# Kernel optimization log

Measured on AMD Instinct MI355X. Metric: run time of the kernel, lower is better.

The kernel has to match this reference:

```python
import jax, jax.numpy as jnp
import numpy as np

B, S, D = 8, 4096, 256
H, DK, DV = 8, 32, 32


def _layer_norm(x, g, b, eps=1e-6):
    mu = jnp.mean(x, axis=-1, keepdims=True)
    var = jnp.mean(jnp.square(x - mu), axis=-1, keepdims=True)
    return (x - mu) * jax.lax.rsqrt(var + eps) * g + b


def setup_inputs() -> dict:
    key = jax.random.key(0)
    ks = jax.random.split(key, 16)
    std = 1.0 / np.sqrt(D)
    p = lambda k, shp: (jax.random.normal(k, shp, jnp.float32) * std)
    return {
        "h": jax.random.normal(ks[0], (B, S, D), jnp.float32),
        "e": jax.random.normal(ks[1], (B, S, D), jnp.float32),
        "s": jax.random.normal(ks[2], (B, D), jnp.float32),
        "sat_wq": p(ks[3], (D, H * DK)), "sat_wk": p(ks[4], (D, H * DK)),
        "sat_wv": p(ks[5], (D, H * DV)), "sat_wo": p(ks[6], (H * DV, D)),
        "sat_g": jnp.ones((D,), jnp.float32), "sat_b": jnp.zeros((D,), jnp.float32),
        "rel_wq": p(ks[7], (D, H * DK)), "rel_wk": p(ks[8], (D, H * DK)),
        "rel_wv": p(ks[9], (D, H * DV)), "rel_wo": p(ks[10], (H * DV, D)),
        "rel_g": jnp.ones((D,), jnp.float32), "rel_b": jnp.zeros((D,), jnp.float32),
    }


def reference(h, e, s, sat_wq, sat_wk, sat_wv, sat_wo, sat_g, sat_b,
              rel_wq, rel_wk, rel_wv, rel_wo, rel_g, rel_b):
    b, sl, d = h.shape
    scale = 1.0 / np.sqrt(DK)

    # ---- build 5-token context: [left, self, right, entity, relay] ----
    hp = jnp.pad(h, ((0, 0), (1, 1), (0, 0)))  # zeros at both ends
    s_exp = jnp.broadcast_to(s[:, None, :], (b, sl, d))
    ctx = jnp.stack([hp[:, :sl], h, hp[:, 2:], e, s_exp], axis=2)  # [B,S,5,D]

    # ---- satellite attention: 1 query vs 5-token context per position ----
    q = (h @ sat_wq).reshape(b, sl, H, DK)
    k = (ctx @ sat_wk).reshape(b, sl, 5, H, DK)
    v = (ctx @ sat_wv).reshape(b, sl, 5, H, DV)
    attn = jax.nn.softmax(jnp.einsum('bshd,bschd->bshc', q, k) * scale, axis=-1)
    o = jnp.einsum('bshc,bschd->bshd', attn, v).reshape(b, sl, H * DV) @ sat_wo
    h_out = _layer_norm(o + h, sat_g, sat_b)  # [B,S,D]

    # ---- relay attention: relay query vs [s; h_out] ----
    s_h = jnp.concatenate([s[:, None, :], h_out], axis=1)  # [B,S+1,D]
    qr = (s @ rel_wq).reshape(b, H, DK)
    kr = (s_h @ rel_wk).reshape(b, sl + 1, H, DK)
    vr = (s_h @ rel_wv).reshape(b, sl + 1, H, DV)
    attn_r = jax.nn.softmax(jnp.einsum('bhd,bkhd->bhk', qr, kr) * scale, axis=-1)
    orl = jnp.einsum('bhk,bkhd->bhd', attn_r, vr).reshape(b, H * DV) @ rel_wo
    s_out = _layer_norm(orl + s, rel_g, rel_b)  # [B,D]

    return (h_out, s_out)
```

## Files before the change

### kernel.cpp

```cpp
#include <hip/hip_runtime.h>
#include <hip/hip_bf16.h>

typedef unsigned short ushort_t;
typedef unsigned int uint_t;
typedef __attribute__((ext_vector_type(8))) short bf16x8;
typedef __attribute__((ext_vector_type(4))) float f32x4;

#define NB 8
#define NS 4096
#define ND 256
#define NH 8
#define NDK 32
#define NBS (NB*NS)
#define NK  (NS+1)
#define CH  513
#define NCH 8
static const size_t PBUF = (size_t)NB*(NS+1)*ND;
static const size_t HSZ  = (size_t)NBS*ND;

__device__ __forceinline__ ushort_t f2b(float x){
  union { __hip_bfloat16 b; ushort_t u; } cv; cv.b = __float2bfloat16(x); return cv.u;
}
__device__ __forceinline__ float b2f(ushort_t u){
  union { uint_t u; float f; } cv; cv.u = ((uint_t)u) << 16; return cv.f;
}
__device__ __forceinline__ void gload16(const ushort_t* g, ushort_t* l){
  __builtin_amdgcn_global_load_lds(
      (const __attribute__((address_space(1))) void*)g,
      (__attribute__((address_space(3))) void*)l, 16, 0, 0);
}
__device__ __forceinline__ uint4 packbf16x8(float4 a, float4 b){
  uint4 p;
  p.x = f2b(a.x) | ((uint_t)f2b(a.y)<<16);
  p.y = f2b(a.z) | ((uint_t)f2b(a.w)<<16);
  p.z = f2b(b.x) | ((uint_t)f2b(b.y)<<16);
  p.w = f2b(b.z) | ((uint_t)f2b(b.w)<<16);
  return p;
}

__device__ __forceinline__ float bsum256(float v){
  __shared__ float tmp[4];
  #pragma unroll
  for (int o=32;o>0;o>>=1) v += __shfl_down(v,o);
  if ((threadIdx.x & 63)==0) tmp[threadIdx.x>>6] = v;
  __syncthreads();
  float r = tmp[0]+tmp[1]+tmp[2]+tmp[3];
  __syncthreads();
  return r;
}

__global__ __launch_bounds__(256) void prep(
    const float* __restrict__ w0, const float* __restrict__ w1, const float* __restrict__ w2,
    const float* __restrict__ w3, const float* __restrict__ w4, const float* __restrict__ w5,
    ushort_t* __restrict__ WtAll,
    const float* __restrict__ s,
    const float* __restrict__ rwq,
    ushort_t* __restrict__ ksb, ushort_t* __restrict__ vsb,
    float* __restrict__ qr, ushort_t* __restrict__ krv)
{
  __shared__ float sh[64*68];
  const int blk = blockIdx.x;
  const int tid = threadIdx.x;
  if (blk < 96){
    const int z = blk >> 4, xy = blk & 15;
    const float* W = (z==0)?w0:(z==1)?w1:(z==2)?w2:(z==3)?w3:(z==4)?w4:w5;
    ushort_t* Wt = WtAll + (size_t)z*65536;
    float (*t)[68] = (float(*)[68])sh;
    const int k0 = (xy>>2)*64, n0 = (xy&3)*64;
    const int tr = tid>>4, tc4 = (tid&15)*4;
    #pragma unroll
    for (int i=0;i<4;i++){
      int r = tr + i*16;
      float4 v = *(const float4*)&W[(size_t)(k0+r)*ND + n0 + tc4];
      t[r][tc4]=v.x; t[r][tc4+1]=v.y; t[r][tc4+2]=v.z; t[r][tc4+3]=v.w;
    }
    __syncthreads();
    #pragma unroll
    for (int i=0;i<4;i++){
      int n = tr + i*16;
      uint_t q0 = f2b(t[tc4+0][n]) | ((uint_t)f2b(t[tc4+1][n])<<16);
      uint_t q1 = f2b(t[tc4+2][n]) | ((uint_t)f2b(t[tc4+3][n])<<16);
      *(uint2*)&Wt[(size_t)(n0+n)*ND + k0 + tc4] = make_uint2(q0,q1);
    }
  } else {
    const int rem = blk - 96;
    const int b = rem & 7, which = rem >> 3;
    const float* W = (which==0)?w1:(which==1)?w2:(which==2)?rwq:(which==3)?w4:w5;
    float* a = sh;
    a[tid] = s[(size_t)b*ND + tid];
    __syncthreads();
    float acc = 0.f;
    #pragma unroll 8
    for (int d=0; d<ND; d++)
      acc = fmaf(a[d], W[(size_t)d*ND + tid], acc);
    switch (which){
      case 0: ksb[(size_t)b*ND + tid] = f2b(acc); break;
      case 1: vsb[(size_t)b*ND + tid] = f2b(acc); break;
      case 2: qr[(size_t)b*ND + tid] = acc; break;
      case 3: krv[(size_t)b*NK*512 + tid] = f2b(acc); break;
      default: krv[(size_t)b*NK*512 + 256 + tid] = f2b(acc); break;
    }
  }
}

__global__ __launch_bounds__(512) void gemm_qkve(const float* __restrict__ hA,
    const float* __restrict__ eA, const ushort_t* __restrict__ Wt,
    ushort_t* __restrict__ hQKV, ushort_t* __restrict__ eKV)
{
  __shared__ __align__(16) ushort_t As[2][128][64];
  __shared__ __align__(16) ushort_t Bs[2][128][64];
  const int y = blockIdx.y;
  const float* A; const ushort_t* Wb; ushort_t* Y; int ldn, col0;
  if (y < 6){ A=hA; Wb=Wt;        Y=hQKV; ldn=768; col0=y*128; }
  else      { A=eA; Wb=Wt+65536;  Y=eKV;  ldn=512; col0=(y-6)*128; }
  const int tid  = threadIdx.x;
  const int row0 = blockIdx.x*128;
  const int lane = tid & 63;
  const int wave = tid >> 6;
  const int wr = (wave>>2)*64;
  const int wc = (wave&3)*32;
  const int l15 = lane & 15, lg = lane >> 4;
  const int lr8 = lane >> 3;
  const int l7  = lane & 7;
  const int ls  = l7 ^ lr8;

  const float* Af = A + (size_t)(row0 + wave*16 + lr8)*ND + l7*8;
  char* AwBase = (char*)&As[0][0][0];
  const int awoff = (wave*16 + lr8)*128 + ((l7 ^ lr8)<<4);
  const ushort_t* Bsrc = Wb + (size_t)(col0 + wave*16 + lr8)*ND + ls*8;

  f32x4 acc[4][2] = {};

  #define STAGE(t, bb) do{ \
    const float* ga = Af + (t)*64; \
    float4 a0=*(const float4*)ga,          a1=*(const float4*)(ga+4); \
    float4 a2=*(const float4*)(ga+8*ND),   a3=*(const float4*)(ga+8*ND+4); \
    *(uint4*)(AwBase + (size_t)(bb)*16384 + awoff)        = packbf16x8(a0,a1); \
    *(uint4*)(AwBase + (size_t)(bb)*16384 + awoff + 1024) = packbf16x8(a2,a3); \
    gload16(Bsrc + (t)*64,                &Bs[bb][wave*16][0]); \
    gload16(Bsrc + (size_t)8*ND + (t)*64, &Bs[bb][wave*16+8][0]); \
  }while(0)
  #define COMPUTE(bb) do{ \
    _Pragma("unroll") \
    for (int ks=0; ks<2; ks++){ \
      bf16x8 af[4], bfr[2]; \
      _Pragma("unroll") \
      for (int mi=0;mi<4;mi++){ \
        int ra = wr + mi*16 + l15; int cb = (ks<<6) + (lg<<4); \
        af[mi] = *(const bf16x8*)((const char*)&As[bb][0][0] + ra*128 + (cb ^ ((ra&7)<<4))); \
      } \
      _Pragma("unroll") \
      for (int ni=0;ni<2;ni++){ \
        int rb = wc + ni*16 + l15; int cb = (ks<<6) + (lg<<4); \
        bfr[ni] = *(const bf16x8*)((const char*)&Bs[bb][0][0] + rb*128 + (cb ^ ((rb&7)<<4))); \
      } \
      _Pragma("unroll") \
      for (int mi=0;mi<4;mi++) \
        _Pragma("unroll") \
        for (int ni=0;ni<2;ni++) \
          acc[mi][ni] = __builtin_amdgcn_mfma_f32_16x16x32_bf16(af[mi], bfr[ni], acc[mi][ni], 0,0,0); \
    } \
  }while(0)

  STAGE(0, 0);
  __syncthreads();
  STAGE(1, 1); COMPUTE(0); __syncthreads();
  STAGE(2, 0); COMPUTE(1); __syncthreads();
  STAGE(3, 1); COMPUTE(0); __syncthreads();
  COMPUTE(1);
  #undef STAGE
  #undef COMPUTE

  #pragma unroll
  for (int mi=0;mi<4;mi++)
    #pragma unroll
    for (int r=0;r<4;r++){
      size_t orow = (size_t)(row0 + wr + mi*16 + lg*4 + r);
      #pragma unroll
      for (int ni=0;ni<2;ni++)
        Y[orow*(size_t)ldn + col0 + wc + ni*16 + l15] = f2b(acc[mi][ni][r]);
    }
}

__global__ __launch_bounds__(512) void gemm_krv(const ushort_t* __restrict__ A,
    const ushort_t* __restrict__ Wt, ushort_t* __restrict__ Y)
{
  __shared__ __align__(16) ushort_t As[2][128][64];
  __shared__ __align__(16) ushort_t Bs[2][128][64];
  const int tid  = threadIdx.x;
  const int row0 = blockIdx.x*128;
  const int col0 = blockIdx.y*128;
  const int lane = tid & 63;
  const int wave = tid >> 6;
  const int wr = (wave>>2)*64;
  const int wc = (wave&3)*32;
  const int l15 = lane & 15, lg = lane >> 4;
  const int lr8 = lane >> 3;
  const int ls  = (lane & 7) ^ lr8;

  const ushort_t* Asrc = A  + (size_t)(row0 + wave*16 + lr8)*ND + ls*8;
  const ushort_t* Bsrc = Wt + (size_t)(col0 + wave*16 + lr8)*ND + ls*8;

  f32x4 acc[4][2] = {};

  #define STAGE(t, bb) do{ \
    gload16(Asrc + (t)*64,                &As[bb][wave*16][0]); \
    gload16(Asrc + (size_t)8*ND + (t)*64, &As[bb][wave*16+8][0]); \
    gload16(Bsrc + (t)*64,                &Bs[bb][wave*16][0]); \
    gload16(Bsrc + (size_t)8*ND + (t)*64, &Bs[bb][wave*16+8][0]); \
  }while(0)
  #define COMPUTE(bb) do{ \
    _Pragma("unroll") \
    for (int ks=0; ks<2; ks++){ \
      bf16x8 af[4], bfr[2]; \
      _Pragma("unroll") \
      for (int mi=0;mi<4;mi++){ \
        int ra = wr + mi*16 + l15; int cb = (ks<<6) + (lg<<4); \
        af[mi] = *(const bf16x8*)((const char*)&As[bb][0][0] + ra*128 + (cb ^ ((ra&7)<<4))); \
      } \
      _Pragma("unroll") \
      for (int ni=0;ni<2;ni++){ \
        int rb = wc + ni*16 + l15; int cb = (ks<<6) + (lg<<4); \
        bfr[ni] = *(const bf16x8*)((const char*)&Bs[bb][0][0] + rb*128 + (cb ^ ((rb&7)<<4))); \
      } \
      _Pragma("unroll") \
      for (int mi=0;mi<4;mi++) \
        _Pragma("unroll") \
        for (int ni=0;ni<2;ni++) \
          acc[mi][ni] = __builtin_amdgcn_mfma_f32_16x16x32_bf16(af[mi], bfr[ni], acc[mi][ni], 0,0,0); \
    } \
  }while(0)

  STAGE(0, 0);
  __syncthreads();
  STAGE(1, 1); COMPUTE(0); __syncthreads();
  STAGE(2, 0); COMPUTE(1); __syncthreads();
  STAGE(3, 1); COMPUTE(0); __syncthreads();
  COMPUTE(1);
  #undef STAGE
  #undef COMPUTE

  #pragma unroll
  for (int mi=0;mi<4;mi++)
    #pragma unroll
    for (int r=0;r<4;r++){
      int row = row0 + wr + mi*16 + lg*4 + r;
      size_t orow = (size_t)(row>>12)*NK + 1 + (row&4095);
      #pragma unroll
      for (int ni=0;ni<2;ni++)
        Y[orow*512 + col0 + wc + ni*16 + l15] = f2b(acc[mi][ni][r]);
    }
}

__global__ __launch_bounds__(512) void oproj_ln(const ushort_t* __restrict__ A,
    const ushort_t* __restrict__ Wt, const float* __restrict__ hres,
    const float* __restrict__ g, const float* __restrict__ bta,
    float* __restrict__ outf, ushort_t* __restrict__ outb)
{
  __shared__ __align__(16) ushort_t As[2][64][64];
  __shared__ float rs[64][4], rq[64][4];
  __shared__ float gl[ND], bl[ND];
  const int tid  = threadIdx.x;
  const int row0 = blockIdx.x*64;
  const int lane = tid & 63;
  const int wave = tid >> 6;
  const int wr = (wave>>2)*32;
  const int wc = (wave&3)*64;
  const int l15 = lane & 15, lg = lane >> 4;
  const int lr8 = lane >> 3;
  const int ls  = (lane & 7) ^ lr8;

  if (tid < ND){ gl[tid] = g[tid]; bl[tid] = bta[tid]; }

  const ushort_t* Asrc = A + (size_t)(row0 + wave*8 + lr8)*ND + ls*8;

  f32x4 acc[2][4] = {};

  #define STAGE3(t, bb) gload16(Asrc + (t)*64, &As[bb][wave*8][0])
  #define COMPUTE3(t, bb) do{ \
    _Pragma("unroll") \
    for (int ks=0; ks<2; ks++){ \
      bf16x8 af[2], bfr[4]; \
      _Pragma("unroll") \
      for (int mi=0;mi<2;mi++){ \
        int ra = wr + mi*16 + l15; int cb = (ks<<6) + (lg<<4); \
        af[mi] = *(const bf16x8*)((const char*)&As[bb][0][0] + ra*128 + (cb ^ ((ra&7)<<4))); \
      } \
      _Pragma("unroll") \
      for (int ni=0;ni<4;ni++) \
        bfr[ni] = *(const bf16x8*)&Wt[(size_t)(wc + ni*16 + l15)*ND + (t)*64 + ks*32 + lg*8]; \
      _Pragma("unroll") \
      for (int mi=0;mi<2;mi++) \
        _Pragma("unroll") \
        for (int ni=0;ni<4;ni++) \
          acc[mi][ni] = __builtin_amdgcn_mfma_f32_16x16x32_bf16(af[mi], bfr[ni], acc[mi][ni], 0,0,0); \
    } \
  }while(0)

  STAGE3(0, 0);
  __syncthreads();
  STAGE3(1, 1); COMPUTE3(0, 0); __syncthreads();
  STAGE3(2, 0); COMPUTE3(1, 1); __syncthreads();
  STAGE3(3, 1); COMPUTE3(2, 0); __syncthreads();
  COMPUTE3(3, 1);
  #undef STAGE3
  #undef COMPUTE3

  #pragma unroll
  for (int mi=0;mi<2;mi++)
    #pragma unroll
    for (int rr=0;rr<4;rr++){
      size_t rowb = (size_t)(row0 + wr + mi*16 + lg*4 + rr)*ND;
      #pragma unroll
      for (int ni=0;ni<4;ni++)
        acc[mi][ni][rr] += hres[rowb + wc + ni*16 + l15];
    }

  #pragma unroll
  for (int mi=0;mi<2;mi++)
    #pragma unroll
    for (int rr=0;rr<4;rr++){
      float sv = 0.f, qv = 0.f;
      #pragma unroll
      for (int ni=0;ni<4;ni++){ float x = acc[mi][ni][rr]; sv += x; qv += x*x; }
      #pragma unroll
      for (int o=1;o<16;o<<=1){ sv += __shfl_xor(sv,o); qv += __shfl_xor(qv,o); }
      if (l15 == 0){
        int rl = wr + mi*16 + lg*4 + rr;
        rs[rl][wave&3] = sv; rq[rl][wave&3] = qv;
      }
    }
  __syncthreads();

  #pragma unroll
  for (int mi=0;mi<2;mi++)
    #pragma unroll
    for (int rr=0;rr<4;rr++){
      int rl = wr + mi*16 + lg*4 + rr;
      float sm = rs[rl][0] + rs[rl][1] + rs[rl][2] + rs[rl][3];
      float sq = rq[rl][0] + rq[rl][1] + rq[rl][2] + rq[rl][3];
      float mu = sm * (1.0f/ND);
      float var = sq * (1.0f/ND) - mu*mu;
      float rstd = rsqrtf(var + 1e-6f);
      size_t rowb = (size_t)(row0 + rl)*ND;
      #pragma unroll
      for (int ni=0;ni<4;ni++){
        int col = wc + ni*16 + l15;
        float yv = (acc[mi][ni][rr] - mu)*rstd*gl[col] + bl[col];
        outf[rowb + col] = yv;
        outb[rowb + col] = f2b(yv);
      }
    }
}

__device__ __forceinline__ void load8(float* d, const ushort_t* p){
  bf16x8 v = *(const bf16x8*)p;
  #pragma unroll
  for (int i=0;i<8;i++) d[i] = b2f((ushort_t)v[i]);
}
__device__ __forceinline__ void zero8(float* d){
  #pragma unroll
  for (int i=0;i<8;i++) d[i] = 0.f;
}
__global__ __launch_bounds__(256) void sat_attn4(const ushort_t* __restrict__ HQ,
    const ushort_t* __restrict__ EKV,
    const ushort_t* __restrict__ KS, const ushort_t* __restrict__ VS,
    ushort_t* __restrict__ O)
{
  const int tid = threadIdx.x;
  const int l  = tid & 3;
  const int g  = tid >> 2;
  const int hh = g & 7;
  const int pi = g >> 3;
  const int pos = blockIdx.x*8 + pi;
  const int b = pos >> 12, t = pos & 4095;
  const int co = hh*NDK + l*8;
  const float scale = 0.17677669529663687f;

  const size_t rq = (size_t)pos*768;
  const size_t re = (size_t)pos*512;
  float q[8], k0[8], k1[8], k2[8], k3[8], k4[8];
  load8(q,  HQ + rq + co);
  load8(k1, HQ + rq + 256 + co);
  load8(k3, EKV + re + co);
  load8(k4, KS + (size_t)b*ND + co);
  if (t > 0)    load8(k0, HQ + rq - 768 + 256 + co);
  else          zero8(k0);
  if (t < NS-1) load8(k2, HQ + rq + 768 + 256 + co);
  else          zero8(k2);

  float s0=0.f,s1=0.f,s2=0.f,s3=0.f,s4=0.f;
  #pragma unroll
  for (int i=0;i<8;i++){
    s0 = fmaf(q[i],k0[i],s0); s1 = fmaf(q[i],k1[i],s1); s2 = fmaf(q[i],k2[i],s2);
    s3 = fmaf(q[i],k3[i],s3); s4 = fmaf(q[i],k4[i],s4);
  }
  #pragma unroll
  for (int mm=1; mm<4; mm<<=1){
    s0 += __shfl_xor(s0,mm); s1 += __shfl_xor(s1,mm); s2 += __shfl_xor(s2,mm);
    s3 += __shfl_xor(s3,mm); s4 += __shfl_xor(s4,mm);
  }
  s0*=scale; s1*=scale; s2*=scale; s3*=scale; s4*=scale;
  float m = fmaxf(fmaxf(fmaxf(s0,s1),fmaxf(s2,s3)),s4);
  float p0=expf(s0-m), p1=expf(s1-m), p2=expf(s2-m), p3=expf(s3-m), p4=expf(s4-m);
  float inv = 1.0f/(p0+p1+p2+p3+p4);

  float v0[8], v1[8], v2[8], v3[8], v4[8];
  load8(v1, HQ + rq + 512 + co);
  load8(v3, EKV + re + 256 + co);
  load8(v4, VS + (size_t)b*ND + co);
  if (t > 0)    load8(v0, HQ + rq - 768 + 512 + co);
  else          zero8(v0);
  if (t < NS-1) load8(v2, HQ + rq + 768 + 512 + co);
  else          zero8(v2);

  float o[8];
  #pragma unroll
  for (int i=0;i<8;i++)
    o[i] = (p0*v0[i] + p1*v1[i] + p2*v2[i] + p3*v3[i] + p4*v4[i]) * inv;
  uint4 pk;
  pk.x = f2b(o[0])|((uint_t)f2b(o[1])<<16);
  pk.y = f2b(o[2])|((uint_t)f2b(o[3])<<16);
  pk.z = f2b(o[4])|((uint_t)f2b(o[5])<<16);
  pk.w = f2b(o[6])|((uint_t)f2b(o[7])<<16);
  *(uint4*)&O[(size_t)pos*ND + co] = pk;
}

__global__ __launch_bounds__(256) void rel_part(const float* __restrict__ QR,
    const ushort_t* __restrict__ KRV,
    float* __restrict__ pO, float* __restrict__ pM, float* __restrict__ pL)
{
  const int bh = blockIdx.x;
  const int b = bh >> 3, h = bh & 7;
  const int c = blockIdx.y;
  const int k0 = c*CH;
  const int kn = min(NK, k0+CH) - k0;
  const int tid = threadIdx.x;
  __shared__ float sc[CH];
  __shared__ float qs[NDK];
  __shared__ float red[8][NDK];
  __shared__ float tmp[4];
  if (tid < NDK) qs[tid] = QR[(size_t)b*ND + h*NDK + tid];
  __syncthreads();
  const float scale = 0.17677669529663687f;
  for (int kk=tid; kk<kn; kk+=256){
    const ushort_t* kp = KRV + ((size_t)b*NK + k0 + kk)*512 + h*NDK;
    float sdot = 0.f;
    #pragma unroll
    for (int w=0; w<4; w++){
      bf16x8 kv = *(const bf16x8*)(kp + w*8);
      #pragma unroll
      for (int i=0;i<8;i++) sdot = fmaf(qs[w*8+i], b2f((ushort_t)kv[i]), sdot);
    }
    sc[kk] = sdot * scale;
  }
  __syncthreads();
  float lm = -1e30f;
  for (int kk=tid; kk<kn; kk+=256) lm = fmaxf(lm, sc[kk]);
  #pragma unroll
  for (int o=32;o>0;o>>=1) lm = fmaxf(lm, __shfl_down(lm,o));
  if ((tid & 63)==0) tmp[tid>>6] = lm;
  __syncthreads();
  float m = fmaxf(fmaxf(tmp[0],tmp[1]),fmaxf(tmp[2],tmp[3]));
  __syncthreads();
  float ls = 0.f;
  for (int kk=tid; kk<kn; kk+=256){ float p = expf(sc[kk]-m); sc[kk] = p; ls += p; }
  #pragma unroll
  for (int o=32;o>0;o>>=1) ls += __shfl_down(ls,o);
  if ((tid & 63)==0) tmp[tid>>6] = ls;
  __syncthreads();
  float lsum = tmp[0]+tmp[1]+tmp[2]+tmp[3];
  int grp = tid>>5, d = tid&31;
  float acc = 0.f;
  for (int kk=grp; kk<kn; kk+=8)
    acc = fmaf(sc[kk], b2f(KRV[((size_t)b*NK + k0 + kk)*512 + 256 + h*NDK + d]), acc);
  red[grp][d] = acc;
  __syncthreads();
  if (grp == 0){
    float tot = 0.f;
    #pragma unroll
    for (int i=0;i<8;i++) tot += red[i][d];
    pO[((size_t)bh*NCH + c)*NDK + d] = tot;
    if (d == 0){ pM[bh*NCH + c] = m; pL[bh*NCH + c] = lsum; }
  }
}

__global__ __launch_bounds__(256) void rel_tail(const float* __restrict__ pO,
    const float* __restrict__ pM, const float* __restrict__ pL,
    const float* __restrict__ WO, const float* __restrict__ Sv,
    const float* __restrict__ g, const float* __restrict__ bta,
    float* __restrict__ out)
{
  const int b = blockIdx.x, j = threadIdx.x;
  __shared__ float ol[ND];
  {
    const int h = j >> 5, d = j & 31;
    const int bh = b*NH + h;
    float m = -1e30f;
    #pragma unroll
    for (int c=0;c<NCH;c++) m = fmaxf(m, pM[bh*NCH + c]);
    float o = 0.f, l = 0.f;
    #pragma unroll
    for (int c=0;c<NCH;c++){
      float w = expf(pM[bh*NCH + c] - m);
      o = fmaf(pO[((size_t)bh*NCH + c)*NDK + d], w, o);
      l = fmaf(pL[bh*NCH + c], w, l);
    }
    ol[j] = o / l;
  }
  __syncthreads();
  float x = 0.f;
  for (int d=0; d<ND; d++) x = fmaf(ol[d], WO[(size_t)d*ND + j], x);
  x += Sv[(size_t)b*ND + j];
  float mu = bsum256(x) * (1.0f/ND);
  float dd = x - mu;
  float var = bsum256(dd*dd) * (1.0f/ND);
  out[(size_t)NBS*ND + (size_t)b*ND + j] = dd * rsqrtf(var + 1e-6f) * g[j] + bta[j];
}

extern "C" void kernel_launch(void* const* d_in, const int* in_sizes, int n_in,
                              void* d_out, int out_size, void* d_ws, size_t ws_size,
                              hipStream_t stream)
{
  const float* h      = (const float*)d_in[0];
  const float* e      = (const float*)d_in[1];
  const float* s      = (const float*)d_in[2];
  const float* sat_wq = (const float*)d_in[3];
  const float* sat_wk = (const float*)d_in[4];
  const float* sat_wv = (const float*)d_in[5];
  const float* sat_wo = (const float*)d_in[6];
  const float* sat_g  = (const float*)d_in[7];
  const float* sat_b  = (const float*)d_in[8];
  const float* rel_wq = (const float*)d_in[9];
  const float* rel_wk = (const float*)d_in[10];
  const float* rel_wv = (const float*)d_in[11];
  const float* rel_wo = (const float*)d_in[12];
  const float* rel_g  = (const float*)d_in[13];
  const float* rel_b  = (const float*)d_in[14];
  float* out = (float*)d_out;

  float* ws = (float*)d_ws;
  ushort_t* hQKV = (ushort_t*)ws;
  ushort_t* eKV  = (ushort_t*)(ws + 2*PBUF);
  ushort_t* krv  = (ushort_t*)(ws + 4*PBUF);
  ushort_t* hb   = (ushort_t*)(ws + 5*PBUF);
  ushort_t* satO = hb + HSZ;
  ushort_t* Wt   = satO + HSZ;
  float* smalls  = (float*)(Wt + 6*65536);
  ushort_t* ksb = (ushort_t*)smalls;
  ushort_t* vsb = ksb + 2048;
  float* qr  = smalls + 4096;
  float* pO  = smalls + 8192;
  float* pM  = pO + (size_t)NB*NH*NCH*NDK;
  float* pL  = pM + NB*NH*NCH;

  dim3 gb(256);

  prep<<<136, gb, 0, stream>>>(sat_wq, sat_wk, sat_wv, sat_wo, rel_wk, rel_wv, Wt,
                               s, rel_wq, ksb, vsb, qr, krv);

  gemm_qkve<<<dim3(NBS/128, 10), dim3(512), 0, stream>>>(h, e, Wt, hQKV, eKV);

  sat_attn4<<<NBS/8, gb, 0, stream>>>(hQKV, eKV, ksb, vsb, satO);

  oproj_ln<<<NBS/64, dim3(512), 0, stream>>>(satO, Wt + 3*65536, h, sat_g, sat_b, out, hb);

  gemm_krv<<<dim3(NBS/128, 4), dim3(512), 0, stream>>>(hb, Wt + 4*65536, krv);

  rel_part<<<dim3(NB*NH, NCH), gb, 0, stream>>>(qr, krv, pO, pM, pL);

  rel_tail<<<NB, gb, 0, stream>>>(pO, pM, pL, rel_wo, s, rel_g, rel_b, out);
}
```

Measured before the change: 175.3 us.

## Keep full-K A row block resident in LDS and loop over all output columns

The QKV/E-KV projection GEMM now has each block load a 64-row slice of h or e once, convert it to bf16 and keep all 256 K columns in LDS. The block then walks every output column tile (6 for h, 4 for e) while double-buffering only the weight tiles. Before, each of up to 10 column blocks re-read and re-converted the same fp32 activation rows from global memory. The cost is a smaller 64x128 tile per step with fewer MFMAs per LDS load, fewer blocks (1024), a serial loop over column tiles, and a sync on every step.

```diff
diff --git a/kernel.cpp b/kernel.cpp
--- a/kernel.cpp
+++ b/kernel.cpp
@@ -107,79 +107,94 @@
     const float* __restrict__ eA, const ushort_t* __restrict__ Wt,
     ushort_t* __restrict__ hQKV, ushort_t* __restrict__ eKV)
 {
-  __shared__ __align__(16) ushort_t As[2][128][64];
+  __shared__ __align__(16) ushort_t Ap[64][256];
   __shared__ __align__(16) ushort_t Bs[2][128][64];
-  const int y = blockIdx.y;
-  const float* A; const ushort_t* Wb; ushort_t* Y; int ldn, col0;
-  if (y < 6){ A=hA; Wb=Wt;        Y=hQKV; ldn=768; col0=y*128; }
-  else      { A=eA; Wb=Wt+65536;  Y=eKV;  ldn=512; col0=(y-6)*128; }
-  const int tid  = threadIdx.x;
-  const int row0 = blockIdx.x*128;
+  const int blk = blockIdx.x;
+  const bool isH = blk < 512;
+  const float* A = isH ? hA : eA;
+  const ushort_t* Wb = isH ? Wt : (Wt + 65536);
+  ushort_t* Y = isH ? hQKV : eKV;
+  const int ldn  = isH ? 768 : 512;
+  const int ncol = isH ? 6 : 4;
+  const int row0 = (blk & 511) * 64;
+  const int tid = threadIdx.x;
   const int lane = tid & 63;
   const int wave = tid >> 6;
-  const int wr = (wave>>2)*64;
-  const int wc = (wave&3)*32;
+  const int wr  = (wave>>2)*32;
+  const int wcw = (wave&3)*32;
   const int l15 = lane & 15, lg = lane >> 4;
   const int lr8 = lane >> 3;
-  const int l7  = lane & 7;
-  const int ls  = l7 ^ lr8;
-
-  const float* Af = A + (size_t)(row0 + wave*16 + lr8)*ND + l7*8;
-  char* AwBase = (char*)&As[0][0][0];
-  const int awoff = (wave*16 + lr8)*128 + ((l7 ^ lr8)<<4);
-  const ushort_t* Bsrc = Wb + (size_t)(col0 + wave*16 + lr8)*ND + ls*8;
-
-  f32x4 acc[4][2] = {};
-
-  #define STAGE(t, bb) do{ \
-    const float* ga = Af + (t)*64; \
-    float4 a0=*(const float4*)ga,          a1=*(const float4*)(ga+4); \
-    float4 a2=*(const float4*)(ga+8*ND),   a3=*(const float4*)(ga+8*ND+4); \
-    *(uint4*)(AwBase + (size_t)(bb)*16384 + awoff)        = packbf16x8(a0,a1); \
-    *(uint4*)(AwBase + (size_t)(bb)*16384 + awoff + 1024) = packbf16x8(a2,a3); \
-    gload16(Bsrc + (t)*64,                &Bs[bb][wave*16][0]); \
-    gload16(Bsrc + (size_t)8*ND + (t)*64, &Bs[bb][wave*16+8][0]); \
+  const int ls  = (lane & 7) ^ lr8;
+
+  #pragma unroll
+  for (int i=0;i<4;i++){
+    int sgi = tid + i*512;
+    int r   = sgi >> 5;
+    int c8  = (sgi & 31) * 8;
+    const float* ga = A + (size_t)(row0 + r)*ND + c8;
+    float4 a0 = *(const float4*)ga, a1 = *(const float4*)(ga+4);
+    int byte = r*512 + ((c8*2) ^ ((r&7)<<4));
+    *(uint4*)((char*)&Ap[0][0] + byte) = packbf16x8(a0,a1);
+  }
+
+  const ushort_t* Bbase = Wb + (size_t)(wave*16 + lr8)*ND + ls*8;
+  #define STAGEB(ct, kt, bb) do{ \
+    const ushort_t* bp = Bbase + (size_t)(ct)*128*ND + (kt)*64; \
+    gload16(bp,                &Bs[bb][wave*16][0]); \
+    gload16(bp + (size_t)8*ND, &Bs[bb][wave*16+8][0]); \
   }while(0)
-  #define COMPUTE(bb) do{ \
-    _Pragma("unroll") \
-    for (int ks=0; ks<2; ks++){ \
-      bf16x8 af[4], bfr[2]; \
-      _Pragma("unroll") \
-      for (int mi=0;mi<4;mi++){ \
-        int ra = wr + mi*16 + l15; int cb = (ks<<6) + (lg<<4); \
-        af[mi] = *(const bf16x8*)((const char*)&As[bb][0][0] + ra*128 + (cb ^ ((ra&7)<<4))); \
-      } \
-      _Pragma("unroll") \
-      for (int ni=0;ni<2;ni++){ \
-        int rb = wc + ni*16 + l15; int cb = (ks<<6) + (lg<<4); \
-        bfr[ni] = *(const bf16x8*)((const char*)&Bs[bb][0][0] + rb*128 + (cb ^ ((rb&7)<<4))); \
-      } \
-      _Pragma("unroll") \
-      for (int mi=0;mi<4;mi++) \
-        _Pragma("unroll") \
-        for (int ni=0;ni<2;ni++) \
-          acc[mi][ni] = __builtin_amdgcn_mfma_f32_16x16x32_bf16(af[mi], bfr[ni], acc[mi][ni], 0,0,0); \
-    } \
-  }while(0)
-
-  STAGE(0, 0);
-  __syncthreads();
-  STAGE(1, 1); COMPUTE(0); __syncthreads();
-  STAGE(2, 0); COMPUTE(1); __syncthreads();
-  STAGE(3, 1); COMPUTE(0); __syncthreads();
-  COMPUTE(1);
-  #undef STAGE
-  #undef COMPUTE
-
-  #pragma unroll
-  for (int mi=0;mi<4;mi++)
-    #pragma unroll
-    for (int r=0;r<4;r++){
-      size_t orow = (size_t)(row0 + wr + mi*16 + lg*4 + r);
-      #pragma unroll
-      for (int ni=0;ni<2;ni++)
-        Y[orow*(size_t)ldn + col0 + wc + ni*16 + l15] = f2b(acc[mi][ni][r]);
-    }
+
+  const f32x4 vzero = {0.f,0.f,0.f,0.f};
+  f32x4 acc[2][2] = {};
+  STAGEB(0,0,0);
+  __syncthreads();
+  int buf = 0;
+  const int total = ncol*4;
+  for (int s = 0; s < total; ++s){
+    const int kt = s & 3;
+    if (s+1 < total) STAGEB((s+1)>>2, (s+1)&3, buf^1);
+    #pragma unroll
+    for (int ks=0; ks<2; ks++){
+      bf16x8 af[2], bfr[2];
+      #pragma unroll
+      for (int mi=0;mi<2;mi++){
+        int ra  = wr + mi*16 + l15;
+        int cb2 = kt*128 + ks*64 + lg*16;
+        af[mi] = *(const bf16x8*)((const char*)&Ap[0][0] + ra*512 + (cb2 ^ ((ra&7)<<4)));
+      }
+      #pragma unroll
+      for (int ni=0;ni<2;ni++){
+        int rb = wcw + ni*16 + l15;
+        int cb = (ks<<6) + (lg<<4);
+        bfr[ni] = *(const bf16x8*)((const char*)&Bs[buf][0][0] + rb*128 + (cb ^ ((rb&7)<<4)));
+      }
+      #pragma unroll
+      for (int mi=0;mi<2;mi++)
+        #pragma unroll
+        for (int ni=0;ni<2;ni++)
+          acc[mi][ni] = __builtin_amdgcn_mfma_f32_16x16x32_bf16(af[mi], bfr[ni], acc[mi][ni], 0,0,0);
+    }
+    __syncthreads();
+    buf ^= 1;
+    if (kt == 3){
+      const int col0 = (s >> 2) * 128;
+      #pragma unroll
+      for (int mi=0;mi<2;mi++)
+        #pragma unroll
+        for (int r=0;r<4;r++){
+          size_t orow = (size_t)(row0 + wr + mi*16 + lg*4 + r);
+          #pragma unroll
+          for (int ni=0;ni<2;ni++)
+            Y[orow*(size_t)ldn + col0 + wcw + ni*16 + l15] = f2b(acc[mi][ni][r]);
+        }
+      #pragma unroll
+      for (int mi=0;mi<2;mi++)
+        #pragma unroll
+        for (int ni=0;ni<2;ni++)
+          acc[mi][ni] = vzero;
+    }
+  }
+  #undef STAGEB
 }
 
 __global__ __launch_bounds__(512) void gemm_krv(const ushort_t* __restrict__ A,
@@ -559,7 +574,7 @@
   prep<<<136, gb, 0, stream>>>(sat_wq, sat_wk, sat_wv, sat_wo, rel_wk, rel_wv, Wt,
                                s, rel_wq, ksb, vsb, qr, krv);
 
-  gemm_qkve<<<dim3(NBS/128, 10), dim3(512), 0, stream>>>(h, e, Wt, hQKV, eKV);
+  gemm_qkve<<<1024, dim3(512), 0, stream>>>(h, e, Wt, hQKV, eKV);
 
   sat_attn4<<<NBS/8, gb, 0, stream>>>(hQKV, eKV, ksb, vsb, satO);
 
```

After: 172.3 us. No clear change (-1.7%).
